# Kernel optimization log

Hardware: AMD Instinct MI355X
Metric: run time of the kernel (lower is better)

Reference implementation:

```python
import jax, jax.numpy as jnp
import numpy as np

B, L = 8, 1024
VOCAB, D_ENC, D_MAIN = 260, 128, 256
N_ENC, N_MAIN, N_DEC, N_HEADS = 3, 6, 3, 4
N_RATIO = 6.0  # 1/target_ratio
NEG = jnp.float32(-1e9)


def setup_inputs() -> dict:
    key = jax.random.key(0)
    kc = iter(jax.random.split(key, 40))
    def nrm(shape, std):
        return jax.random.normal(next(kc), shape, jnp.float32) * std
    inp = {'byte_ids': jax.random.randint(next(kc), (B, L), 0, VOCAB)}
    inp['embed'] = nrm((VOCAB, D_ENC), D_ENC ** -0.5)
    eye = jnp.eye(D_ENC, dtype=jnp.float32)
    inp['wq'] = eye + nrm((D_ENC, D_ENC), 0.02)  # init is identity in the torch module
    inp['wk'] = eye + nrm((D_ENC, D_ENC), 0.02)
    inp['proj_up'] = nrm((D_MAIN, D_ENC), D_ENC ** -0.5)
    inp['proj_down'] = nrm((D_ENC, D_MAIN), 1e-3)
    inp['norm_w'] = jnp.ones((D_ENC,), jnp.float32)
    inp['norm_b'] = jnp.zeros((D_ENC,), jnp.float32)
    for pre, n, d in [('enc', N_ENC, D_ENC), ('main', N_MAIN, D_MAIN), ('dec', N_DEC, D_ENC)]:
        inp[pre + '_ln1_w'] = jnp.ones((n, d), jnp.float32)
        inp[pre + '_ln1_b'] = jnp.zeros((n, d), jnp.float32)
        inp[pre + '_qkv'] = nrm((n, 3 * d, d), d ** -0.5)   # MHA in_proj (3D, D)
        inp[pre + '_wo'] = nrm((n, d, d), d ** -0.5)        # MHA out_proj
        inp[pre + '_ln2_w'] = jnp.ones((n, d), jnp.float32)
        inp[pre + '_ln2_b'] = jnp.zeros((n, d), jnp.float32)
        inp[pre + '_w1'] = nrm((n, 2 * d, d), d ** -0.5)    # mlp_mult = 2
        inp[pre + '_w2'] = nrm((n, d, 2 * d), (2 * d) ** -0.5)
    return inp


def _ln(x, w, b):
    mu = jnp.mean(x, axis=-1, keepdims=True)
    var = jnp.mean((x - mu) ** 2, axis=-1, keepdims=True)
    return (x - mu) * jax.lax.rsqrt(var + 1e-5) * w + b


def _mha(x, wqkv, wo, bias):
    Bb, S, D = x.shape
    dh = D // N_HEADS
    q, k, v = jnp.split(x @ wqkv.T, 3, axis=-1)
    q = q.reshape(Bb, S, N_HEADS, dh)
    k = k.reshape(Bb, S, N_HEADS, dh)
    v = v.reshape(Bb, S, N_HEADS, dh)
    scores = jnp.einsum('bqhd,bkhd->bhqk', q, k) * (dh ** -0.5) + bias
    attn = jax.nn.softmax(scores, axis=-1)
    out = jnp.einsum('bhqk,bkhd->bqhd', attn, v).reshape(Bb, S, D)
    return out @ wo.T


def _block(x, stack, i, bias):
    ln1w, ln1b, qkv, wo, ln2w, ln2b, w1, w2 = (a[i] for a in stack)
    x = x + _mha(_ln(x, ln1w, ln1b), qkv, wo, bias)
    h = _ln(x, ln2w, ln2b)
    return x + jax.nn.gelu(h @ w1.T, approximate=False) @ w2.T


def _downsample(x, b_hard):
    # scatter boundary tokens to the front of a padded (B, S, D) buffer
    Bb, S, D = x.shape
    idx = jnp.cumsum(b_hard, axis=1).astype(jnp.int32) - 1
    dest = jnp.where(b_hard > 0.5, idx, S)  # S is out-of-range -> dropped
    def sc(xb, db):
        return jnp.zeros((S, D), xb.dtype).at[db].set(xb, mode='drop')
    out = jax.vmap(sc)(x, dest)
    counts = jnp.sum(b_hard, axis=1).astype(jnp.int32)
    mask = jnp.arange(S)[None, :] < counts[:, None]
    return out, mask


def _forward(byte_ids, embed, wq, wk,
             enc_ln1_w, enc_ln1_b, enc_qkv, enc_wo, enc_ln2_w, enc_ln2_b, enc_w1, enc_w2,
             proj_up,
             main_ln1_w, main_ln1_b, main_qkv, main_wo, main_ln2_w, main_ln2_b, main_w1, main_w2,
             proj_down,
             dec_ln1_w, dec_ln1_b, dec_qkv, dec_wo, dec_ln2_w, dec_ln2_b, dec_w1, dec_w2,
             norm_w, norm_b):
    causal = jnp.where(jnp.triu(jnp.ones((L, L), bool), 1), NEG, jnp.float32(0.0))[None, None]
    x = embed[byte_ids]  # (B, L, D_ENC)
    enc_p = (enc_ln1_w, enc_ln1_b, enc_qkv, enc_wo, enc_ln2_w, enc_ln2_b, enc_w1, enc_w2)
    for i in range(N_ENC):
        x = _block(x, enc_p, i, causal)

    # --- dynamic chunking (routing + ratio loss) ---
    def l2n(t):
        return t / jnp.maximum(jnp.linalg.norm(t, axis=-1, keepdims=True), 1e-12)
    q = l2n(x @ wq.T)
    k = l2n(x @ wk.T)
    k_prev = jnp.pad(k[:, :-1], ((0, 0), (1, 0), (0, 0)))
    cos = jnp.sum(q * k_prev, axis=-1)
    p = jnp.clip(0.5 * (1.0 - cos), 0.0, 1.0)
    p = jnp.concatenate([jnp.ones_like(p[:, :1]), p[:, 1:]], axis=1)
    b_hard = (p >= 0.5).astype(jnp.float32)
    N = N_RATIO
    F_act = jnp.mean(b_hard)
    G_act = jnp.mean(p)
    ratio_loss = N / (N - 1.0) * ((N - 1.0) * F_act * G_act + (1.0 - F_act) * (1.0 - G_act))
    compressed, comp_mask = _downsample(x, b_hard)
    p_comp = _downsample(p[..., None], b_hard)[0][..., 0]

    # --- main stack on compressed sequence (padded to L, masked) ---
    z = compressed @ proj_up.T
    main_bias = causal + jnp.where(comp_mask, jnp.float32(0.0), NEG)[:, None, None, :]
    main_p = (main_ln1_w, main_ln1_b, main_qkv, main_wo, main_ln2_w, main_ln2_b, main_w1, main_w2)
    for i in range(N_MAIN):
        z = _block(z, main_p, i, main_bias)
    z = z @ proj_down.T  # (B, L, D_ENC)

    # --- chunk-level EMA (parallel linear-recurrence scan) + gather + STE ---
    p_c = jnp.clip(p_comp, 1e-4, 1.0 - 1e-4)
    a = (1.0 - p_c).at[:, 0].set(0.0)[..., None]          # z_bar[0] = z[0]
    bv = (p_c[..., None] * z).at[:, :1].set(z[:, :1])
    def comb(lhs, rhs):
        al, bl = lhs
        ar, br = rhs
        return (al * ar, ar * bl + br)
    z_bar = jax.lax.associative_scan(comb, (a, bv), axis=1)[1]
    chunk_idx = jnp.clip(jnp.cumsum(b_hard, axis=1).astype(jnp.int32) - 1, 0, None)
    z_up = jnp.take_along_axis(z_bar, jnp.broadcast_to(chunk_idx[:, :, None], z_bar.shape), axis=1)
    c = b_hard * p + (1.0 - b_hard) * (1.0 - p)
    c_ste = c + jax.lax.stop_gradient(1.0 - c)
    x = x + c_ste[..., None] * z_up

    dec_p = (dec_ln1_w, dec_ln1_b, dec_qkv, dec_wo, dec_ln2_w, dec_ln2_b, dec_w1, dec_w2)
    for i in range(N_DEC):
        x = _block(x, dec_p, i, causal)
    x = _ln(x, norm_w, norm_b)
    logits = x @ embed.T  # tied head
    return logits, ratio_loss


def reference(byte_ids, embed, wq, wk,
              enc_ln1_w, enc_ln1_b, enc_qkv, enc_wo, enc_ln2_w, enc_ln2_b, enc_w1, enc_w2,
              proj_up,
              main_ln1_w, main_ln1_b, main_qkv, main_wo, main_ln2_w, main_ln2_b, main_w1, main_w2,
              proj_down,
              dec_ln1_w, dec_ln1_b, dec_qkv, dec_wo, dec_ln2_w, dec_ln2_b, dec_w1, dec_w2,
              norm_w, norm_b):
    return _forward(byte_ids, embed, wq, wk,
                    enc_ln1_w, enc_ln1_b, enc_qkv, enc_wo, enc_ln2_w, enc_ln2_b, enc_w1, enc_w2,
                    proj_up,
                    main_ln1_w, main_ln1_b, main_qkv, main_wo, main_ln2_w, main_ln2_b, main_w1, main_w2,
                    proj_down,
                    dec_ln1_w, dec_ln1_b, dec_qkv, dec_wo, dec_ln2_w, dec_ln2_b, dec_w1, dec_w2,
                    norm_w, norm_b)
```

## Files before the change

### kernel.cpp

```cpp
#include <hip/hip_runtime.h>
#include <hip/hip_bf16.h>

#define B_ 8
#define L_ 1024
#define BL (B_*L_)
#define DENC 128
#define DMAIN 256
#define VOCAB 260
#define NHEADS 4

typedef __hip_bfloat16 bf16;
typedef _Float16 f16;
typedef f16 half8 __attribute__((ext_vector_type(8)));
typedef f16 half4 __attribute__((ext_vector_type(4)));
typedef f16 half2v __attribute__((ext_vector_type(2)));
typedef float f32x4 __attribute__((ext_vector_type(4)));

__global__ __launch_bounds__(64) void k_detect(const void* __restrict__ emb, int* __restrict__ flag){
    int lane = threadIdx.x;
    const unsigned short* u = (const unsigned short*)emb;
    int bad = 0;
    #pragma unroll
    for (int j = 0; j < 4; j++){
        unsigned short h = u[lane + 64*j];
        bf16 t = *(const bf16*)&h;
        float v = __bfloat162float(t);
        if (!(fabsf(v) < 1e4f)) bad++;
    }
    #pragma unroll
    for (int o = 32; o >= 1; o >>= 1) bad += __shfl_xor(bad, o);
    if (lane == 0) flag[0] = (bad == 0) ? 1 : 0;
}

struct CvtArgs {
    const void* src[31];
    unsigned offs[32];
};
__global__ void k_cvt_all(CvtArgs a, float* __restrict__ dst, f16* __restrict__ dst16,
                          int total, const int* __restrict__ flag){
    int isbf = flag[0];
    for (int i = blockIdx.x*256 + threadIdx.x; i < total; i += gridDim.x*256){
        int lo = 0, hi = 30;
        while (lo < hi){ int mid = (lo+hi+1)>>1; if (a.offs[mid] <= (unsigned)i) lo = mid; else hi = mid-1; }
        int j = i - (int)a.offs[lo];
        float v = isbf ? __bfloat162float(((const bf16*)a.src[lo])[j])
                       : ((const float*)a.src[lo])[j];
        dst[i] = v;
        dst16[i] = (f16)v;
    }
}

__global__ void k_embed(const int* __restrict__ ids, const float* __restrict__ emb, float* __restrict__ x){
    int i = blockIdx.x*256 + threadIdx.x;
    int row = i >> 7, d = i & 127;
    x[i] = emb[ids[row]*DENC + d];
}

template<int D>
__global__ __launch_bounds__(256) void k_ln16(const float* __restrict__ x, const float* __restrict__ w,
                                              const float* __restrict__ b, f16* __restrict__ y){
    int row = blockIdx.x*4 + (threadIdx.x >> 6);
    int lane = threadIdx.x & 63;
    const float* xr = x + (size_t)row*D;
    float v[D/64];
    float s = 0.f;
    #pragma unroll
    for (int j=0;j<D/64;j++){ v[j] = xr[lane + j*64]; s += v[j]; }
    #pragma unroll
    for (int o=32;o>=1;o>>=1) s += __shfl_xor(s,o);
    float mu = s / (float)D;
    float s2 = 0.f;
    #pragma unroll
    for (int j=0;j<D/64;j++){ float dd = v[j]-mu; s2 += dd*dd; }
    #pragma unroll
    for (int o=32;o>=1;o>>=1) s2 += __shfl_xor(s2,o);
    float inv = rsqrtf(s2/(float)D + 1e-5f);
    f16* yr = y + (size_t)row*D;
    #pragma unroll
    for (int j=0;j<D/64;j++){
        int d = lane + j*64;
        yr[d] = (f16)((v[j]-mu)*inv*w[d] + b[d]);
    }
}

#define GBM 64
#define GBN 64
#define GBK 32
__global__ __launch_bounds__(256) void k_gemm2(const float* __restrict__ A, const float* __restrict__ Wq,
        const float* __restrict__ Wk, float* __restrict__ Cq, float* __restrict__ Ck, int K)
{
    __shared__ float As[GBK][GBM+4];
    __shared__ float Ws[GBK][GBN+4];
    int tid = threadIdx.x;
    int bm = blockIdx.y * GBM;
    int bn = blockIdx.x * GBN;
    int tx = tid & 15, ty = tid >> 4;
    float acc[4][4] = {};
    for (int k0 = 0; k0 < K; k0 += GBK){
        #pragma unroll
        for (int i = tid; i < GBM*GBK; i += 256){
            int m = i >> 5, kk = i & 31;
            As[kk][m] = A[(size_t)(bm+m)*K + k0 + kk];
        }
        #pragma unroll
        for (int i = tid; i < GBN*GBK; i += 256){
            int n = i >> 5, kk = i & 31;
            int gn = bn + n;
            const float* W = (gn < 128) ? Wq : Wk;
            int wr = gn & 127;
            Ws[kk][n] = W[(size_t)wr*K + k0 + kk];
        }
        __syncthreads();
        #pragma unroll
        for (int kk = 0; kk < GBK; kk++){
            float a0[4], w0[4];
            *(float4*)a0 = *(const float4*)&As[kk][ty*4];
            *(float4*)w0 = *(const float4*)&Ws[kk][tx*4];
            #pragma unroll
            for (int i=0;i<4;i++)
                #pragma unroll
                for (int j=0;j<4;j++) acc[i][j] += a0[i]*w0[j];
        }
        __syncthreads();
    }
    #pragma unroll
    for (int i=0;i<4;i++){
        int m = bm + ty*4 + i;
        #pragma unroll
        for (int j=0;j<4;j++){
            int n = bn + tx*4 + j;
            float* C = (n < 128) ? Cq : Ck;
            C[(size_t)m*128 + (n & 127)] = acc[i][j];
        }
    }
}

template<int K>
__global__ __launch_bounds__(256) void k_hgemm(const f16* __restrict__ A, const f16* __restrict__ W,
        const float* __restrict__ R, float* __restrict__ C, f16* __restrict__ C16,
        void* __restrict__ OutRaw, const int* __restrict__ flag, int N, int mode,
        f16* __restrict__ Qd, f16* __restrict__ Kd, f16* __restrict__ Vd,
        int dShift, int dhShift)
{
    __shared__ half8 As[4][64];
    __shared__ half8 Ws[4][64];
    int tid = threadIdx.x;
    int wave = tid >> 6, lane = tid & 63;
    int wr = wave >> 1, wc = wave & 1;
    int quad = lane >> 4, l15 = lane & 15;
    int bm = blockIdx.y * 64, bn = blockIdx.x * 64;

    f32x4 acc[2][2] = {};
    int srow = tid >> 2, sc8 = tid & 3;
    const f16* ap0 = A + (size_t)(bm + srow)*K + sc8*8;
    int gn = bn + srow;
    const f16* wp0 = W + (size_t)gn*K + sc8*8;
    bool wok = (gn < N);

    for (int k0 = 0; k0 < K; k0 += 32){
        __syncthreads();
        As[sc8][srow] = *(const half8*)(ap0 + k0);
        Ws[sc8][srow] = wok ? *(const half8*)(wp0 + k0) : (half8)(f16)0.f;
        __syncthreads();
        half8 af[2], wf[2];
        af[0] = As[quad][wr*32 + l15];
        af[1] = As[quad][wr*32 + 16 + l15];
        wf[0] = Ws[quad][wc*32 + l15];
        wf[1] = Ws[quad][wc*32 + 16 + l15];
        #pragma unroll
        for (int i=0;i<2;i++)
            #pragma unroll
            for (int j=0;j<2;j++)
                acc[i][j] = __builtin_amdgcn_mfma_f32_16x16x32_f16(af[i], wf[j], acc[i][j], 0, 0, 0);
    }

    #pragma unroll
    for (int j=0;j<2;j++){
        int n = bn + wc*32 + j*16 + l15;
        if (n >= N) continue;
        #pragma unroll
        for (int i=0;i<2;i++){
            #pragma unroll
            for (int r=0;r<4;r++){
                int m = bm + wr*32 + i*16 + quad*4 + r;
                float v = acc[i][j][r];
                if (mode == 5){
                    int which = n >> dShift;
                    int rem = n & ((1<<dShift)-1);
                    int hh = rem >> dhShift;
                    int dd = rem & ((1<<dhShift)-1);
                    int bb = m >> 10, tt = m & 1023;
                    int Hn = 1 << (dShift - dhShift);
                    f16* dst = (which==0) ? Qd : ((which==1) ? Kd : Vd);
                    if (which == 2)
                        dst[((((size_t)bb*Hn + hh) << dhShift) + dd)*L_ + tt] = (f16)v;
                    else
                        dst[((((size_t)bb*Hn + hh)*L_ + tt) << dhShift) + dd] = (f16)v;
                    continue;
                }
                size_t off = (size_t)m*N + n;
                if (mode == 1){ C[off] = v + R[off]; }
                else if (mode == 2){
                    v = 0.5f*v*(1.0f + erff(v*0.70710678118654752f));
                    C16[off] = (f16)v;
                } else if (mode == 3){
                    if (flag[0]) ((bf16*)OutRaw)[off] = __float2bfloat16(v);
                    else         ((float*)OutRaw)[off] = v;
                } else C[off] = v;
            }
        }
    }
}

template<int K>
__global__ __launch_bounds__(256) void k_lngemm(const float* __restrict__ A, const f16* __restrict__ W,
        const float* __restrict__ lnw, const float* __restrict__ lnb, int doLN,
        float* __restrict__ C, void* __restrict__ OutRaw,
        const int* __restrict__ flag, int N, int mode)
{
    constexpr int SA = K + 8;
    constexpr int RPT = K/64;
    __shared__ f16 sA[64*SA];
    int tid = threadIdx.x;
    int wave = tid >> 6, lane = tid & 63;
    int wr = wave >> 1, wc = wave & 1;
    int quad = lane >> 4, l15 = lane & 15;
    int bm = blockIdx.y * 64, bn = blockIdx.x * 64;

    float wv_[RPT], bv_[RPT];
    #pragma unroll
    for (int j=0;j<RPT;j++){
        int d = lane*RPT + j;
        wv_[j] = doLN ? lnw[d] : 1.f;
        bv_[j] = doLN ? lnb[d] : 0.f;
    }
    for (int rr=0; rr<16; rr++){
        int row = wave*16 + rr;
        const float* xr = A + (size_t)(bm+row)*K + lane*RPT;
        float v[RPT];
        if (RPT==2){ float2 t = *(const float2*)xr; v[0]=t.x; v[1]=t.y; }
        else       { float4 t = *(const float4*)xr; v[0]=t.x; v[1]=t.y; v[2]=t.z; v[3]=t.w; }
        float mu = 0.f, inv = 1.f;
        if (doLN){
            float s=0.f;
            #pragma unroll
            for (int j=0;j<RPT;j++) s += v[j];
            #pragma unroll
            for (int o=32;o>=1;o>>=1) s += __shfl_xor(s,o);
            mu = s / (float)K;
            float s2=0.f;
            #pragma unroll
            for (int j=0;j<RPT;j++){ float dd=v[j]-mu; s2+=dd*dd; }
            #pragma unroll
            for (int o=32;o>=1;o>>=1) s2 += __shfl_xor(s2,o);
            inv = rsqrtf(s2/(float)K + 1e-5f);
        }
        if (RPT==2){
            half2v h;
            h[0]=(f16)((v[0]-mu)*inv*wv_[0]+bv_[0]);
            h[1]=(f16)((v[1]-mu)*inv*wv_[1]+bv_[1]);
            *(half2v*)&sA[row*SA + lane*2] = h;
        } else {
            half4 h;
            #pragma unroll
            for (int j=0;j<4;j++) h[j]=(f16)((v[j]-mu)*inv*wv_[j]+bv_[j]);
            *(half4*)&sA[row*SA + lane*4] = h;
        }
    }
    __syncthreads();

    f32x4 acc[2][2] = {};
    int n0 = bn + wc*32 + l15;
    bool ok0 = n0 < N, ok1 = (n0+16) < N;
    const f16* w0p = W + (size_t)n0*K + quad*8;
    const f16* w1p = W + (size_t)(n0+16)*K + quad*8;
    #pragma unroll 4
    for (int k0=0;k0<K;k0+=32){
        half8 af[2], wf[2];
        af[0] = *(const half8*)&sA[(wr*32 + l15)*SA + k0 + quad*8];
        af[1] = *(const half8*)&sA[(wr*32 + 16 + l15)*SA + k0 + quad*8];
        wf[0] = ok0 ? *(const half8*)(w0p + k0) : (half8)(f16)0.f;
        wf[1] = ok1 ? *(const half8*)(w1p + k0) : (half8)(f16)0.f;
        #pragma unroll
        for (int i=0;i<2;i++)
            #pragma unroll
            for (int j=0;j<2;j++)
                acc[i][j] = __builtin_amdgcn_mfma_f32_16x16x32_f16(af[i], wf[j], acc[i][j], 0, 0, 0);
    }

    #pragma unroll
    for (int j=0;j<2;j++){
        int n = bn + wc*32 + j*16 + l15;
        if (n >= N) continue;
        #pragma unroll
        for (int i=0;i<2;i++){
            #pragma unroll
            for (int r=0;r<4;r++){
                int m = bm + wr*32 + i*16 + quad*4 + r;
                float v = acc[i][j][r];
                size_t off = (size_t)m*N + n;
                if (mode == 3){
                    if (flag[0]) ((bf16*)OutRaw)[off] = __float2bfloat16(v);
                    else         ((float*)OutRaw)[off] = v;
                } else C[off] = v;
            }
        }
    }
}

template<int DH>
__global__ __launch_bounds__(256) void k_mflash(const f16* __restrict__ Qh, const f16* __restrict__ Kh,
        const f16* __restrict__ Vt, f16* __restrict__ out, const int* __restrict__ counts,
        float scale)
{
    constexpr int BQ = 64, BK = 64;
    constexpr int RS = DH + 8;
    constexpr int PS = BK + 8;
    __shared__ f16 sQ[BQ*RS];
    __shared__ f16 sK[BK*RS];
    __shared__ f16 sVt[DH*PS];
    __shared__ f16 sP[BQ*PS];

    int x = blockIdx.x, b = x >> 2, h = x & 3;
    int yy = blockIdx.y;
    int qt = (yy < 8) ? yy : 23 - yy;
    int q0 = qt * BQ;
    int tid = threadIdx.x;
    int wv = tid >> 6, lane = tid & 63;
    int quad = lane >> 4, l15 = lane & 15;

    const f16* Qb = Qh + (size_t)x*L_*DH;
    const f16* Kb = Kh + (size_t)x*L_*DH;
    const f16* Vb = Vt + (size_t)x*DH*L_;
    int kcap = counts ? counts[b] : L_;
    int klen = min(kcap, q0 + BQ);

    for (int i = tid; i < BQ*DH/8; i += 256){
        int r = (8*i)/DH, c = (8*i)%DH;
        *(half8*)&sQ[r*RS + c] = *(const half8*)&Qb[(size_t)(q0+r)*DH + c];
    }

    float m[4], l[4];
    #pragma unroll
    for (int r=0;r<4;r++){ m[r] = -1e30f; l[r] = 0.f; }
    f32x4 accO[DH/16] = {};

    for (int k0 = 0; k0 < klen; k0 += BK){
        __syncthreads();
        for (int i = tid; i < BK*DH/8; i += 256){
            int r = (8*i)/DH, c = (8*i)%DH;
            *(half8*)&sK[r*RS + c] = *(const half8*)&Kb[(size_t)(k0+r)*DH + c];
        }
        for (int i = tid; i < DH*BK/8; i += 256){
            int r = (8*i)/BK, c = (8*i)%BK;
            *(half8*)&sVt[r*PS + c] = *(const half8*)&Vb[(size_t)r*L_ + k0 + c];
        }
        __syncthreads();

        half8 af[DH/32];
        #pragma unroll
        for (int ds=0; ds<DH/32; ds++)
            af[ds] = *(const half8*)&sQ[(16*wv + l15)*RS + quad*8 + 32*ds];
        f32x4 accS[4] = {};
        #pragma unroll
        for (int t=0;t<4;t++){
            #pragma unroll
            for (int ds=0; ds<DH/32; ds++){
                half8 bf = *(const half8*)&sK[(16*t + l15)*RS + quad*8 + 32*ds];
                accS[t] = __builtin_amdgcn_mfma_f32_16x16x32_f16(af[ds], bf, accS[t], 0, 0, 0);
            }
        }

        #pragma unroll
        for (int r=0;r<4;r++){
            int qrow = q0 + 16*wv + quad*4 + r;
            float sv[4];
            #pragma unroll
            for (int t=0;t<4;t++){
                float v = accS[t][r]*scale;
                int kp = k0 + 16*t + l15;
                if (kp > qrow || kp >= kcap) v = -1e30f;
                sv[t] = v;
            }
            float rm = fmaxf(fmaxf(sv[0],sv[1]), fmaxf(sv[2],sv[3]));
            rm = fmaxf(rm, __shfl_xor(rm, 1));
            rm = fmaxf(rm, __shfl_xor(rm, 2));
            rm = fmaxf(rm, __shfl_xor(rm, 4));
            rm = fmaxf(rm, __shfl_xor(rm, 8));
            float mn = fmaxf(m[r], rm);
            float al = __expf(m[r] - mn);
            float p0 = __expf(sv[0]-mn), p1 = __expf(sv[1]-mn);
            float p2 = __expf(sv[2]-mn), p3 = __expf(sv[3]-mn);
            float rs = p0+p1+p2+p3;
            rs += __shfl_xor(rs, 1);
            rs += __shfl_xor(rs, 2);
            rs += __shfl_xor(rs, 4);
            rs += __shfl_xor(rs, 8);
            l[r] = l[r]*al + rs;
            m[r] = mn;
            #pragma unroll
            for (int dt=0; dt<DH/16; dt++) accO[dt][r] *= al;
            int prow = 16*wv + quad*4 + r;
            sP[prow*PS + 16*0 + l15] = (f16)p0;
            sP[prow*PS + 16*1 + l15] = (f16)p1;
            sP[prow*PS + 16*2 + l15] = (f16)p2;
            sP[prow*PS + 16*3 + l15] = (f16)p3;
        }

        half8 pf[2];
        #pragma unroll
        for (int ks=0; ks<2; ks++)
            pf[ks] = *(const half8*)&sP[(16*wv + l15)*PS + quad*8 + 32*ks];
        #pragma unroll
        for (int dt=0; dt<DH/16; dt++){
            #pragma unroll
            for (int ks=0; ks<2; ks++){
                half8 bv = *(const half8*)&sVt[(16*dt + l15)*PS + quad*8 + 32*ks];
                accO[dt] = __builtin_amdgcn_mfma_f32_16x16x32_f16(pf[ks], bv, accO[dt], 0, 0, 0);
            }
        }
    }

    #pragma unroll
    for (int r=0;r<4;r++){
        float inv = 1.0f / l[r];
        int qrow = q0 + 16*wv + quad*4 + r;
        #pragma unroll
        for (int dt=0; dt<DH/16; dt++){
            int d = 16*dt + l15;
            out[((size_t)b*L_ + qrow)*(NHEADS*DH) + h*DH + d] = (f16)(accO[dt][r]*inv);
        }
    }
}

__global__ __launch_bounds__(64) void k_router(const float* __restrict__ Q, const float* __restrict__ Kr,
        float* __restrict__ p, float* __restrict__ bh)
{
    int idx = blockIdx.x;
    int t = idx & (L_-1);
    int lane = threadIdx.x;
    float pv;
    if (t == 0){ pv = 1.0f; }
    else {
        const float* qr = Q  + (size_t)idx*DENC;
        const float* kr = Kr + (size_t)(idx-1)*DENC;
        float qq=0.f, kk=0.f, qk=0.f;
        #pragma unroll
        for (int j=0;j<2;j++){
            float qv = qr[lane + j*64], kv = kr[lane + j*64];
            qq += qv*qv; kk += kv*kv; qk += qv*kv;
        }
        #pragma unroll
        for (int o=32;o>=1;o>>=1){ qq += __shfl_xor(qq,o); kk += __shfl_xor(kk,o); qk += __shfl_xor(qk,o); }
        float cosv = qk / (fmaxf(sqrtf(qq),1e-12f)*fmaxf(sqrtf(kk),1e-12f));
        pv = 0.5f*(1.0f - cosv);
        pv = fminf(fmaxf(pv, 0.0f), 1.0f);
    }
    if (lane == 0){ p[idx] = pv; bh[idx] = (pv >= 0.5f) ? 1.0f : 0.0f; }
}

__global__ __launch_bounds__(64) void k_seq(const float* __restrict__ bh, int* __restrict__ cidx,
                      int* __restrict__ src, int* __restrict__ counts, float* __restrict__ acc){
    int b = blockIdx.x;
    int lane = threadIdx.x;
    if (b == 0 && lane < 8) acc[lane] = 0.f;
    int base = b*L_ + lane*16;
    int h[16];
    int cnt = 0;
    #pragma unroll
    for (int j=0;j<16;j++){ h[j] = bh[base+j] > 0.5f; cnt += h[j]; }
    int inc = cnt;
    #pragma unroll
    for (int o=1;o<64;o<<=1){ int nb = __shfl_up(inc, o); if (lane >= o) inc += nb; }
    int run = inc - cnt;
    #pragma unroll
    for (int j=0;j<16;j++){
        run += h[j];
        int ci = run - 1; if (ci < 0) ci = 0;
        cidx[base+j] = ci;
        if (h[j]) src[b*L_ + run-1] = lane*16 + j;
    }
    if (lane == 63) counts[b] = inc;
}

__global__ __launch_bounds__(128) void k_scatter2(const float* __restrict__ x, const float* __restrict__ p,
        const int* __restrict__ src, const int* __restrict__ counts,
        f16* __restrict__ comp, float* __restrict__ pcomp)
{
    int s = blockIdx.x & (L_-1), b = blockIdx.x >> 10, d = threadIdx.x;
    int cnt = counts[b];
    f16* crow = comp + ((size_t)b*L_ + s)*DENC;
    if (s < cnt){
        int t = src[b*L_ + s];
        crow[d] = (f16)x[((size_t)b*L_ + t)*DENC + d];
        if (d == 0) pcomp[b*L_ + s] = p[b*L_ + t];
    } else {
        crow[d] = (f16)0.f;
        if (d == 0) pcomp[b*L_ + s] = 0.f;
    }
}

__global__ __launch_bounds__(256) void k_reduce(const float* __restrict__ p, const float* __restrict__ bh,
                                                float* __restrict__ acc){
    __shared__ float sp[256], sb[256];
    int tid = threadIdx.x;
    float s1=0.f, s2=0.f;
    for (int i = blockIdx.x*256 + tid; i < BL; i += gridDim.x*256){ s1 += p[i]; s2 += bh[i]; }
    sp[tid]=s1; sb[tid]=s2; __syncthreads();
    for (int o=128;o>=1;o>>=1){ if (tid<o){ sp[tid]+=sp[tid+o]; sb[tid]+=sb[tid+o]; } __syncthreads(); }
    if (tid==0){ atomicAdd(&acc[0], sp[0]); atomicAdd(&acc[1], sb[0]); }
}

__global__ __launch_bounds__(256) void k_ema2(const float* __restrict__ z, const float* __restrict__ pcomp,
                                              float* __restrict__ zbar){
    __shared__ float sp[L_];
    int blk = blockIdx.x;
    int b = blk >> 5;
    int tid = threadIdx.x, wv = tid >> 6, lane = tid & 63;
    int d = ((blk & 31) << 2) + wv;
    for (int i = tid; i < L_; i += 256){
        float pc = pcomp[b*L_ + i];
        sp[i] = fminf(fmaxf(pc, 1e-4f), 1.0f - 1e-4f);
    }
    __syncthreads();
    const float* zb = z + ((size_t)b*L_)*DENC + d;
    int t0 = lane*16;
    float zv[16];
    #pragma unroll
    for (int i=0;i<16;i++) zv[i] = zb[(size_t)(t0+i)*DENC];
    float A = 1.f, Bv = 0.f;
    #pragma unroll
    for (int i=0;i<16;i++){
        int t = t0 + i;
        float pc = sp[t];
        float a  = (t==0) ? 0.f : (1.f - pc);
        float bb = (t==0) ? zv[i] : pc*zv[i];
        A = a*A;
        Bv = a*Bv + bb;
    }
    #pragma unroll
    for (int off=1; off<64; off<<=1){
        float Ap = __shfl_up(A, off);
        float Bp = __shfl_up(Bv, off);
        if (lane >= off){ Bv = A*Bp + Bv; A = A*Ap; }
    }
    float sin_ = __shfl_up(Bv, 1);
    if (lane == 0) sin_ = 0.f;
    float s = sin_;
    float* ob = zbar + ((size_t)b*L_)*DENC + d;
    #pragma unroll
    for (int i=0;i<16;i++){
        int t = t0 + i;
        float pc = sp[t];
        float a  = (t==0) ? 0.f : (1.f - pc);
        float bb = (t==0) ? zv[i] : pc*zv[i];
        s = a*s + bb;
        ob[(size_t)t*DENC] = s;
    }
}

__global__ void k_combine(float* __restrict__ x, const float* __restrict__ zbar, const int* __restrict__ cidx){
    int i = blockIdx.x*256 + threadIdx.x;
    int row = i >> 7, d = i & 127;
    int b = row >> 10;
    int ci = cidx[row];
    x[i] += zbar[((size_t)b*L_ + ci)*DENC + d];
}

__global__ void k_loss(const float* __restrict__ acc, void* __restrict__ out, const int* __restrict__ flag){
    float G = acc[0] / (float)BL;
    float F = acc[1] / (float)BL;
    float ratio = 1.2f*(5.0f*F*G + (1.0f-F)*(1.0f-G));
    if (flag[0]) ((bf16*)out)[(size_t)BL*VOCAB] = __float2bfloat16(ratio);
    else         ((float*)out)[(size_t)BL*VOCAB] = ratio;
}

extern "C" void kernel_launch(void* const* d_in, const int* in_sizes, int n_in,
                              void* d_out, int out_size, void* d_ws, size_t ws_size,
                              hipStream_t stream) {
    (void)out_size; (void)ws_size;
    const int* byte_ids = (const int*)d_in[0];

    float* ws = (float*)d_ws;
    size_t off = 0;
    int* FLAG = (int*)ws; off += 16;
    float* W32 = ws + off;

    k_detect<<<1, 64, 0, stream>>>(d_in[1], FLAG);

    CvtArgs ca;
    const float* w32[32];
    unsigned woff = 0;
    for (int i = 1; i < n_in && i < 32; i++){
        w32[i] = W32 + woff;
        ca.src[i-1] = d_in[i];
        ca.offs[i-1] = woff;
        woff += (unsigned)in_sizes[i];
    }
    ca.offs[31] = woff;
    off += woff;
    f16* W16h = (f16*)(ws + off); off += (woff+1)/2;
    const f16* w16[32];
    for (int i = 1; i < n_in && i < 32; i++) w16[i] = W16h + ca.offs[i-1];
    k_cvt_all<<<2048, 256, 0, stream>>>(ca, W32, W16h, (int)woff, FLAG);

    const float* embed    = w32[1];
    const float* wq       = w32[2];
    const float* wk       = w32[3];
    const float* norm_w   = w32[6];
    const float* norm_b   = w32[7];

    float* X    = ws + off; off += (size_t)BL*DENC;
    float* QKVf = ws + off; off += (size_t)BL*3*DMAIN;
    float* ATTf = ws + off; off += (size_t)BL*DMAIN;
    float* Hf   = ws + off; off += (size_t)BL*2*DMAIN;
    float* LNf  = ws + off; off += (size_t)BL*DMAIN;
    float* Z    = ws + off; off += (size_t)BL*DMAIN;
    float* COMPf= ws + off; off += (size_t)BL*DENC;
    float* P    = ws + off; off += BL;
    float* BH   = ws + off; off += BL;
    float* PCOMP= ws + off; off += BL;
    float* ACC  = ws + off; off += 8;
    int* CIDX   = (int*)(ws + off); off += BL;
    int* SRC    = (int*)(ws + off); off += BL;
    int* COUNTS = (int*)(ws + off); off += 64;

    f16* QKV16 = (f16*)QKVf;
    f16* ATT16 = (f16*)ATTf;
    f16* H16   = (f16*)Hf;
    f16* LN16  = (f16*)LNf;
    f16* COMP16= (f16*)COMPf;
    float* Qr  = ATTf;
    float* Kr  = Hf;
    float* ZDN = QKVf;
    float* ZBAR= QKVf + (size_t)BL*DENC;

    auto hgemm = [&](int K, const f16* A, const f16* W, const float* R, float* C, f16* C16,
                     void* Ob, int N, int mode, f16* Qd, f16* Kd, f16* Vd, int dS, int dhS){
        dim3 g((N+63)/64, BL/64);
        if (K == 128)      k_hgemm<128><<<g, 256, 0, stream>>>(A, W, R, C, C16, Ob, FLAG, N, mode, Qd, Kd, Vd, dS, dhS);
        else if (K == 256) k_hgemm<256><<<g, 256, 0, stream>>>(A, W, R, C, C16, Ob, FLAG, N, mode, Qd, Kd, Vd, dS, dhS);
        else               k_hgemm<512><<<g, 256, 0, stream>>>(A, W, R, C, C16, Ob, FLAG, N, mode, Qd, Kd, Vd, dS, dhS);
    };

    auto block128 = [&](float* Xs, const float* l1w, const float* l1b, const f16* qkvw, const f16* wo,
                        const float* l2w, const float* l2b, const f16* w1, const f16* w2){
        k_ln16<128><<<BL/4,256,0,stream>>>(Xs, l1w, l1b, LN16);
        hgemm(128, LN16, qkvw, nullptr, nullptr, nullptr, nullptr, 3*DENC, 5,
              QKV16, QKV16 + (size_t)BL*DENC, QKV16 + (size_t)2*BL*DENC, 7, 5);
        k_mflash<32><<<dim3(B_*NHEADS,16),256,0,stream>>>(QKV16, QKV16 + (size_t)BL*DENC,
                                                          QKV16 + (size_t)2*BL*DENC,
                                                          ATT16, nullptr, 0.17677669529663687f);
        hgemm(128, ATT16, wo, Xs, Xs, nullptr, nullptr, DENC, 1, nullptr, nullptr, nullptr, 0, 0);
        k_ln16<128><<<BL/4,256,0,stream>>>(Xs, l2w, l2b, LN16);
        hgemm(128, LN16, w1, nullptr, nullptr, H16, nullptr, 2*DENC, 2, nullptr, nullptr, nullptr, 0, 0);
        hgemm(256, H16, w2, Xs, Xs, nullptr, nullptr, DENC, 1, nullptr, nullptr, nullptr, 0, 0);
    };
    auto block_main = [&](float* Xs, const float* l1w, const float* l1b, const f16* qkvw, const f16* wo,
                          const float* l2w, const float* l2b, const f16* w1, const f16* w2){
        k_ln16<256><<<BL/4,256,0,stream>>>(Xs, l1w, l1b, LN16);
        hgemm(256, LN16, qkvw, nullptr, nullptr, nullptr, nullptr, 3*DMAIN, 5,
              QKV16, QKV16 + (size_t)BL*DMAIN, QKV16 + (size_t)2*BL*DMAIN, 8, 6);
        k_mflash<64><<<dim3(B_*NHEADS,16),256,0,stream>>>(QKV16, QKV16 + (size_t)BL*DMAIN,
                                                          QKV16 + (size_t)2*BL*DMAIN,
                                                          ATT16, COUNTS, 0.125f);
        hgemm(256, ATT16, wo, Xs, Xs, nullptr, nullptr, DMAIN, 1, nullptr, nullptr, nullptr, 0, 0);
        k_ln16<256><<<BL/4,256,0,stream>>>(Xs, l2w, l2b, LN16);
        hgemm(256, LN16, w1, nullptr, nullptr, H16, nullptr, 2*DMAIN, 2, nullptr, nullptr, nullptr, 0, 0);
        hgemm(512, H16, w2, Xs, Xs, nullptr, nullptr, DMAIN, 1, nullptr, nullptr, nullptr, 0, 0);
    };

    k_embed<<<BL*DENC/256, 256, 0, stream>>>(byte_ids, embed, X);
    for (int i = 0; i < 3; i++)
        block128(X, w32[8] + i*DENC, w32[9] + i*DENC, w16[10] + (size_t)i*3*DENC*DENC,
                 w16[11] + (size_t)i*DENC*DENC, w32[12] + i*DENC, w32[13] + i*DENC,
                 w16[14] + (size_t)i*2*DENC*DENC, w16[15] + (size_t)i*2*DENC*DENC);

    k_gemm2<<<dim3(4, BL/64), 256, 0, stream>>>(X, wq, wk, Qr, Kr, DENC);
    k_router<<<BL, 64, 0, stream>>>(Qr, Kr, P, BH);
    k_seq<<<B_, 64, 0, stream>>>(BH, CIDX, SRC, COUNTS, ACC);
    k_scatter2<<<BL, 128, 0, stream>>>(X, P, SRC, COUNTS, COMP16, PCOMP);
    k_reduce<<<8, 256, 0, stream>>>(P, BH, ACC);

    hgemm(128, COMP16, w16[4], nullptr, Z, nullptr, nullptr, DMAIN, 0, nullptr, nullptr, nullptr, 0, 0);
    for (int i = 0; i < 6; i++)
        block_main(Z, w32[16] + i*DMAIN, w32[17] + i*DMAIN, w16[18] + (size_t)i*3*DMAIN*DMAIN,
                   w16[19] + (size_t)i*DMAIN*DMAIN, w32[20] + i*DMAIN, w32[21] + i*DMAIN,
                   w16[22] + (size_t)i*2*DMAIN*DMAIN, w16[23] + (size_t)i*2*DMAIN*DMAIN);
    k_lngemm<256><<<dim3(2, BL/64), 256, 0, stream>>>(Z, w16[5], nullptr, nullptr, 0,
                                                      ZDN, nullptr, FLAG, DENC, 0);

    k_ema2<<<256, 256, 0, stream>>>(ZDN, PCOMP, ZBAR);
    k_combine<<<BL*DENC/256, 256, 0, stream>>>(X, ZBAR, CIDX);

    for (int i = 0; i < 3; i++)
        block128(X, w32[24] + i*DENC, w32[25] + i*DENC, w16[26] + (size_t)i*3*DENC*DENC,
                 w16[27] + (size_t)i*DENC*DENC, w32[28] + i*DENC, w32[29] + i*DENC,
                 w16[30] + (size_t)i*2*DENC*DENC, w16[31] + (size_t)i*2*DENC*DENC);

    k_lngemm<128><<<dim3(5, BL/64), 256, 0, stream>>>(X, w16[1], norm_w, norm_b, 1,
                                                      nullptr, d_out, FLAG, VOCAB, 3);
    k_loss<<<1,1,0,stream>>>(ACC, d_out, FLAG);
}
```

Measured before the change: 1.216 ms.

## Double GEMM k-tile, fold reduction into k_seq, skip unused fp32 weight copies

The f16 MFMA GEMM now stages a 64-wide K slice per iteration, doing two MFMA k-steps per barrier pair, which halves the sync and loop overhead. The separate k_reduce launch is removed: k_seq sums the probabilities and boundary counts per sequence and adds them atomically, and zeroing of the accumulator moves into k_router. The weight conversion kernel gets a bitmask so it writes fp32 copies only for tensors that need them. The costs are more shared memory per block and reliance on the mask matching which fp32 weights are actually read.

```diff
diff --git a/kernel.cpp b/kernel.cpp
--- a/kernel.cpp
+++ b/kernel.cpp
@@ -37,7 +37,7 @@
     unsigned offs[32];
 };
 __global__ void k_cvt_all(CvtArgs a, float* __restrict__ dst, f16* __restrict__ dst16,
-                          int total, const int* __restrict__ flag){
+                          int total, const int* __restrict__ flag, unsigned f32mask){
     int isbf = flag[0];
     for (int i = blockIdx.x*256 + threadIdx.x; i < total; i += gridDim.x*256){
         int lo = 0, hi = 30;
@@ -45,7 +45,7 @@
         int j = i - (int)a.offs[lo];
         float v = isbf ? __bfloat162float(((const bf16*)a.src[lo])[j])
                        : ((const float*)a.src[lo])[j];
-        dst[i] = v;
+        if ((f32mask >> lo) & 1u) dst[i] = v;
         dst16[i] = (f16)v;
     }
 }
@@ -142,8 +142,8 @@
         f16* __restrict__ Qd, f16* __restrict__ Kd, f16* __restrict__ Vd,
         int dShift, int dhShift)
 {
-    __shared__ half8 As[4][64];
-    __shared__ half8 Ws[4][64];
+    __shared__ half8 As[8][64];
+    __shared__ half8 Ws[8][64];
     int tid = threadIdx.x;
     int wave = tid >> 6, lane = tid & 63;
     int wr = wave >> 1, wc = wave & 1;
@@ -151,27 +151,35 @@
     int bm = blockIdx.y * 64, bn = blockIdx.x * 64;
 
     f32x4 acc[2][2] = {};
-    int srow = tid >> 2, sc8 = tid & 3;
-    const f16* ap0 = A + (size_t)(bm + srow)*K + sc8*8;
-    int gn = bn + srow;
-    const f16* wp0 = W + (size_t)gn*K + sc8*8;
-    bool wok = (gn < N);
-
-    for (int k0 = 0; k0 < K; k0 += 32){
+    int srow = tid >> 3;
+    int sch  = tid & 7;
+    const f16* ap0 = A + (size_t)(bm + srow)*K + sch*8;
+    const f16* ap1 = A + (size_t)(bm + srow + 32)*K + sch*8;
+    int gn0 = bn + srow, gn1 = bn + srow + 32;
+    const f16* wp0 = W + (size_t)gn0*K + sch*8;
+    const f16* wp1 = W + (size_t)gn1*K + sch*8;
+    bool wok0 = gn0 < N, wok1 = gn1 < N;
+
+    for (int k0 = 0; k0 < K; k0 += 64){
         __syncthreads();
-        As[sc8][srow] = *(const half8*)(ap0 + k0);
-        Ws[sc8][srow] = wok ? *(const half8*)(wp0 + k0) : (half8)(f16)0.f;
+        As[sch][srow]      = *(const half8*)(ap0 + k0);
+        As[sch][srow + 32] = *(const half8*)(ap1 + k0);
+        Ws[sch][srow]      = wok0 ? *(const half8*)(wp0 + k0) : (half8)(f16)0.f;
+        Ws[sch][srow + 32] = wok1 ? *(const half8*)(wp1 + k0) : (half8)(f16)0.f;
         __syncthreads();
-        half8 af[2], wf[2];
-        af[0] = As[quad][wr*32 + l15];
-        af[1] = As[quad][wr*32 + 16 + l15];
-        wf[0] = Ws[quad][wc*32 + l15];
-        wf[1] = Ws[quad][wc*32 + 16 + l15];
-        #pragma unroll
-        for (int i=0;i<2;i++)
-            #pragma unroll
-            for (int j=0;j<2;j++)
-                acc[i][j] = __builtin_amdgcn_mfma_f32_16x16x32_f16(af[i], wf[j], acc[i][j], 0, 0, 0);
+        #pragma unroll
+        for (int ks = 0; ks < 2; ks++){
+            half8 af[2], wf[2];
+            af[0] = As[ks*4 + quad][wr*32 + l15];
+            af[1] = As[ks*4 + quad][wr*32 + 16 + l15];
+            wf[0] = Ws[ks*4 + quad][wc*32 + l15];
+            wf[1] = Ws[ks*4 + quad][wc*32 + 16 + l15];
+            #pragma unroll
+            for (int i=0;i<2;i++)
+                #pragma unroll
+                for (int j=0;j<2;j++)
+                    acc[i][j] = __builtin_amdgcn_mfma_f32_16x16x32_f16(af[i], wf[j], acc[i][j], 0, 0, 0);
+        }
     }
 
     #pragma unroll
@@ -434,11 +442,12 @@
 }
 
 __global__ __launch_bounds__(64) void k_router(const float* __restrict__ Q, const float* __restrict__ Kr,
-        float* __restrict__ p, float* __restrict__ bh)
+        float* __restrict__ p, float* __restrict__ bh, float* __restrict__ acc)
 {
     int idx = blockIdx.x;
     int t = idx & (L_-1);
     int lane = threadIdx.x;
+    if (idx == 0 && lane < 8) acc[lane] = 0.f;
     float pv;
     if (t == 0){ pv = 1.0f; }
     else {
@@ -459,16 +468,17 @@
     if (lane == 0){ p[idx] = pv; bh[idx] = (pv >= 0.5f) ? 1.0f : 0.0f; }
 }
 
-__global__ __launch_bounds__(64) void k_seq(const float* __restrict__ bh, int* __restrict__ cidx,
-                      int* __restrict__ src, int* __restrict__ counts, float* __restrict__ acc){
+__global__ __launch_bounds__(64) void k_seq(const float* __restrict__ bh, const float* __restrict__ p,
+                      int* __restrict__ cidx, int* __restrict__ src, int* __restrict__ counts,
+                      float* __restrict__ acc){
     int b = blockIdx.x;
     int lane = threadIdx.x;
-    if (b == 0 && lane < 8) acc[lane] = 0.f;
     int base = b*L_ + lane*16;
     int h[16];
     int cnt = 0;
-    #pragma unroll
-    for (int j=0;j<16;j++){ h[j] = bh[base+j] > 0.5f; cnt += h[j]; }
+    float ps = 0.f;
+    #pragma unroll
+    for (int j=0;j<16;j++){ h[j] = bh[base+j] > 0.5f; cnt += h[j]; ps += p[base+j]; }
     int inc = cnt;
     #pragma unroll
     for (int o=1;o<64;o<<=1){ int nb = __shfl_up(inc, o); if (lane >= o) inc += nb; }
@@ -480,6 +490,10 @@
         cidx[base+j] = ci;
         if (h[j]) src[b*L_ + run-1] = lane*16 + j;
     }
+    float cs = (float)cnt;
+    #pragma unroll
+    for (int o=32;o>=1;o>>=1){ ps += __shfl_xor(ps,o); cs += __shfl_xor(cs,o); }
+    if (lane == 0){ atomicAdd(&acc[0], ps); atomicAdd(&acc[1], cs); }
     if (lane == 63) counts[b] = inc;
 }
 
@@ -500,17 +514,6 @@
     }
 }
 
-__global__ __launch_bounds__(256) void k_reduce(const float* __restrict__ p, const float* __restrict__ bh,
-                                                float* __restrict__ acc){
-    __shared__ float sp[256], sb[256];
-    int tid = threadIdx.x;
-    float s1=0.f, s2=0.f;
-    for (int i = blockIdx.x*256 + tid; i < BL; i += gridDim.x*256){ s1 += p[i]; s2 += bh[i]; }
-    sp[tid]=s1; sb[tid]=s2; __syncthreads();
-    for (int o=128;o>=1;o>>=1){ if (tid<o){ sp[tid]+=sp[tid+o]; sb[tid]+=sb[tid+o]; } __syncthreads(); }
-    if (tid==0){ atomicAdd(&acc[0], sp[0]); atomicAdd(&acc[1], sb[0]); }
-}
-
 __global__ __launch_bounds__(256) void k_ema2(const float* __restrict__ z, const float* __restrict__ pcomp,
                                               float* __restrict__ zbar){
     __shared__ float sp[L_];
@@ -602,7 +605,7 @@
     f16* W16h = (f16*)(ws + off); off += (woff+1)/2;
     const f16* w16[32];
     for (int i = 1; i < n_in && i < 32; i++) w16[i] = W16h + ca.offs[i-1];
-    k_cvt_all<<<2048, 256, 0, stream>>>(ca, W32, W16h, (int)woff, FLAG);
+    k_cvt_all<<<2048, 256, 0, stream>>>(ca, W32, W16h, (int)woff, FLAG, 0x199999E7u);
 
     const float* embed    = w32[1];
     const float* wq       = w32[2];
@@ -638,9 +641,9 @@
     auto hgemm = [&](int K, const f16* A, const f16* W, const float* R, float* C, f16* C16,
                      void* Ob, int N, int mode, f16* Qd, f16* Kd, f16* Vd, int dS, int dhS){
         dim3 g((N+63)/64, BL/64);
-        if (K == 128)      k_hgemm<128><<<g, 256, 0, stream>>>(A, W, R, C, C16, Ob, FLAG, N, mode, Qd, Kd, Vd, dS, dhS);
-        else if (K == 256) k_hgemm<256><<<g, 256, 0, stream>>>(A, W, R, C, C16, Ob, FLAG, N, mode, Qd, Kd, Vd, dS, dhS);
-        else               k_hgemm<512><<<g, 256, 0, stream>>>(A, W, R, C, C16, Ob, FLAG, N, mode, Qd, Kd, Vd, dS, dhS);
+        if (K == 128)      k_hgemm<128><<<g,256,0,stream>>>(A, W, R, C, C16, Ob, FLAG, N, mode, Qd, Kd, Vd, dS, dhS);
+        else if (K == 256) k_hgemm<256><<<g,256,0,stream>>>(A, W, R, C, C16, Ob, FLAG, N, mode, Qd, Kd, Vd, dS, dhS);
+        else               k_hgemm<512><<<g,256,0,stream>>>(A, W, R, C, C16, Ob, FLAG, N, mode, Qd, Kd, Vd, dS, dhS);
     };
 
     auto block128 = [&](float* Xs, const float* l1w, const float* l1b, const f16* qkvw, const f16* wo,
@@ -677,10 +680,9 @@
                  w16[14] + (size_t)i*2*DENC*DENC, w16[15] + (size_t)i*2*DENC*DENC);
 
     k_gemm2<<<dim3(4, BL/64), 256, 0, stream>>>(X, wq, wk, Qr, Kr, DENC);
-    k_router<<<BL, 64, 0, stream>>>(Qr, Kr, P, BH);
-    k_seq<<<B_, 64, 0, stream>>>(BH, CIDX, SRC, COUNTS, ACC);
+    k_router<<<BL, 64, 0, stream>>>(Qr, Kr, P, BH, ACC);
+    k_seq<<<B_, 64, 0, stream>>>(BH, P, CIDX, SRC, COUNTS, ACC);
     k_scatter2<<<BL, 128, 0, stream>>>(X, P, SRC, COUNTS, COMP16, PCOMP);
-    k_reduce<<<8, 256, 0, stream>>>(P, BH, ACC);
 
     hgemm(128, COMP16, w16[4], nullptr, Z, nullptr, nullptr, DMAIN, 0, nullptr, nullptr, nullptr, 0, 0);
     for (int i = 0; i < 6; i++)
```

Result: slower. 1.257 ms (+3.5%).
